# Kernel optimization log

Measured on AMD Instinct MI355X. Metric: run time of the kernel, lower is better.

Reference implementation:

```python
import jax, jax.numpy as jnp
import numpy as np

WS = 7          # window size
NH = 12         # num heads
DIM = 384
HID = 4 * DIM
EPS = 1e-5


def _rel_pos_index(ws):
    coords = np.stack(np.meshgrid(np.arange(ws), np.arange(ws), indexing='ij'))  # (2,ws,ws)
    cf = coords.reshape(2, -1)
    rel = cf[:, :, None] - cf[:, None, :]           # (2,N,N)
    rel = rel.transpose(1, 2, 0)                    # (N,N,2)
    rel[:, :, 0] += ws - 1
    rel[:, :, 1] += ws - 1
    rel[:, :, 0] *= 2 * ws - 1
    return jnp.asarray(rel.sum(-1))                 # (N,N) int

REL_IDX = _rel_pos_index(WS)


def _layernorm(x, g, b):
    m = x.mean(-1, keepdims=True)
    v = ((x - m) ** 2).mean(-1, keepdims=True)
    return (x - m) * jax.lax.rsqrt(v + EPS) * g + b


def setup_inputs() -> dict:
    key = jax.random.key(0)
    ks = jax.random.split(key, 16)
    B, H, W = 8, 112, 112
    s = lambda fan: 1.0 / np.sqrt(fan)
    return {
        'x': jax.random.normal(ks[0], (B, DIM, H, W), jnp.float32),
        'g1': jnp.ones((DIM,), jnp.float32),
        'b1': jnp.zeros((DIM,), jnp.float32),
        'w_qkv': jax.random.normal(ks[1], (DIM, 3 * DIM), jnp.float32) * s(DIM),
        'b_qkv': jnp.zeros((3 * DIM,), jnp.float32),
        'rpb': jax.random.normal(ks[2], ((2 * WS - 1) ** 2, NH), jnp.float32) * 0.02,
        'w_proj': jax.random.normal(ks[3], (DIM, DIM), jnp.float32) * s(DIM),
        'b_proj': jnp.zeros((DIM,), jnp.float32),
        'g2': jnp.ones((DIM,), jnp.float32),
        'b2': jnp.zeros((DIM,), jnp.float32),
        'w_fc1': jax.random.normal(ks[4], (DIM, HID), jnp.float32) * s(DIM),
        'b_fc1': jnp.zeros((HID,), jnp.float32),
        'w_fc2': jax.random.normal(ks[5], (HID, DIM), jnp.float32) * s(HID),
        'b_fc2': jnp.zeros((DIM,), jnp.float32),
    }


def reference(x, g1, b1, w_qkv, b_qkv, rpb, w_proj, b_proj, g2, b2, w_fc1, b_fc1, w_fc2, b_fc2):
    B, C, H, W = x.shape
    x = x.transpose(0, 2, 3, 1)                     # (B,H,W,C)
    shortcut = x
    xn = _layernorm(x, g1, b1)

    # window partition (with padding, no-op when divisible)
    pad_h = (-H) % WS
    pad_w = (-W) % WS
    if pad_h or pad_w:
        xn = jnp.pad(xn, ((0, 0), (0, pad_h), (0, pad_w), (0, 0)))
    Hp, Wp = H + pad_h, W + pad_w
    N = WS * WS
    xw = xn.reshape(B, Hp // WS, WS, Wp // WS, WS, C).transpose(0, 1, 3, 2, 4, 5)
    xw = xw.reshape(-1, N, C)                       # (B_, N, C)
    B_ = xw.shape[0]
    hd = C // NH

    qkv = (xw @ w_qkv + b_qkv).reshape(B_, N, 3, NH, hd)
    q = qkv[:, :, 0].transpose(0, 2, 1, 3) * (hd ** -0.5)   # (B_,h,N,d)
    k = qkv[:, :, 1].transpose(0, 2, 1, 3)
    v = qkv[:, :, 2].transpose(0, 2, 1, 3)

    attn = jnp.einsum('bhnd,bhmd->bhnm', q, k)
    bias = rpb[REL_IDX.reshape(-1)].reshape(N, N, NH).transpose(2, 0, 1)  # (h,N,N)
    attn = jax.nn.softmax(attn + bias[None], axis=-1)

    out = jnp.einsum('bhnm,bhmd->bhnd', attn, v).transpose(0, 2, 1, 3).reshape(B_, N, C)
    out = out @ w_proj + b_proj

    # window reverse
    out = out.reshape(B, Hp // WS, Wp // WS, WS, WS, C).transpose(0, 1, 3, 2, 4, 5)
    out = out.reshape(B, Hp, Wp, C)[:, :H, :W]

    x = shortcut + out
    h = _layernorm(x, g2, b2)
    h = jax.nn.gelu(h @ w_fc1 + b_fc1, approximate=False) @ w_fc2 + b_fc2
    x = x + h
    return x.transpose(0, 3, 1, 2)                  # (B,C,H,W)
```

## Files before the change

### kernel.cpp

```cpp
#include <hip/hip_runtime.h>
#include <cstdint>
#include <cmath>

using u16 = unsigned short;

typedef __bf16 bf16x8 __attribute__((ext_vector_type(8)));
typedef float  f32x4  __attribute__((ext_vector_type(4)));

__device__ __forceinline__ float b2f(u16 u) {
    return __uint_as_float(((unsigned int)u) << 16);
}
__device__ __forceinline__ u16 f2b(float f) {
    unsigned int x = __float_as_uint(f);
    unsigned int r = (x + 0x7fffu + ((x >> 16) & 1u)) >> 16;
    return (u16)r;
}

__device__ __forceinline__ void gload16(const u16* g, u16* l) {
    __builtin_amdgcn_global_load_lds((__attribute__((address_space(1))) void*)g,
                                     (__attribute__((address_space(3))) void*)l,
                                     16, 0, 0);
}

#define LGKM0_FENCE() do { \
    asm volatile("s_waitcnt lgkmcnt(0)" ::: "memory"); \
    __builtin_amdgcn_sched_barrier(0); } while (0)

__device__ __forceinline__ float gelu_f(float x) {
    float z = fabsf(x) * 0.70710678118f;
    float t = __builtin_amdgcn_rcpf(fmaf(0.3275911f, z, 1.0f));
    float poly = fmaf(fmaf(fmaf(fmaf(1.061405429f, t, -1.453152027f),
                               t, 1.421413741f),
                          t, -0.284496736f),
                     t, 0.254829592f) * t;
    float e = __expf(-z * z);
    float erfv = copysignf(1.0f - poly * e, x);
    return 0.5f * x * (1.0f + erfv);
}

__device__ __forceinline__ int tprime(int b, int hw) {
    int r = hw / 112, c = hw - r * 112;
    int wy = r / 7, iy = r - wy * 7;
    int wx = c / 7, ix = c - wx * 7;
    return (b * 256 + wy * 16 + wx) * 49 + iy * 7 + ix;
}

__global__ void detect_dtype(const unsigned int* __restrict__ x, int* __restrict__ flag) {
    __shared__ int cnt[256];
    int tid = threadIdx.x;
    int c = 0;
#pragma unroll
    for (int i = 0; i < 16; ++i) {
        unsigned int w = x[tid * 16 + i];
        int e = (w >> 23) & 0xFF;
        if (e >= 100 && e <= 150) ++c;
    }
    cnt[tid] = c;
    __syncthreads();
    if (tid == 0) {
        int s = 0;
        for (int i = 0; i < 256; ++i) s += cnt[i];
        flag[0] = (s > 3072) ? 1 : 0;
    }
}

__global__ void convertk(const void* __restrict__ src, u16* __restrict__ dst, int n,
                         const int* __restrict__ flagp) {
    int isf = flagp[0];
    int i = blockIdx.x * 256 + threadIdx.x;
    if (i < n) dst[i] = isf ? f2b(((const float*)src)[i]) : ((const u16*)src)[i];
}

__global__ void build_bias(const u16* __restrict__ crpb, float* __restrict__ bias_exp) {
    int row = blockIdx.x, h = blockIdx.y, col = threadIdx.x;
    float v = -1e30f;
    if (row < 49 && col < 49) {
        int ri = row / 7, rj = row - ri * 7;
        int mi = col / 7, mj = col - mi * 7;
        int idx = ((ri - mi + 6) * 13 + (rj - mj + 6)) * 12 + h;
        v = b2f(crpb[idx]);
    }
    bias_exp[(h * 64 + row) * 64 + col] = v;
}

__global__ void wtrans(const u16* __restrict__ in, u16* __restrict__ out, int K, int N) {
    __shared__ u16 tile[32][33];
    int n0 = blockIdx.x * 32, k0 = blockIdx.y * 32;
    int tx = threadIdx.x & 31, ty = threadIdx.x >> 5;
#pragma unroll
    for (int i = 0; i < 4; ++i)
        tile[ty + i * 8][tx] = in[(size_t)(k0 + ty + i * 8) * N + n0 + tx];
    __syncthreads();
#pragma unroll
    for (int i = 0; i < 4; ++i)
        out[(size_t)(n0 + ty + i * 8) * K + k0 + tx] = tile[tx][ty + i * 8];
}

__global__ void ln1_stats(const void* __restrict__ x, float* __restrict__ mean,
                          float* __restrict__ rstd, const int* __restrict__ flagp) {
    int isf = flagp[0];
    int t = blockIdx.x * 256 + threadIdx.x;
    int b = t / 12544, hw = t - b * 12544;
    size_t base = (size_t)b * 384 * 12544 + hw;
    float s = 0.f, sq = 0.f;
    if (isf) {
        const float* p = (const float*)x + base;
        for (int c = 0; c < 384; ++c) {
            float v = p[(size_t)c * 12544];
            s += v; sq += v * v;
        }
    } else {
        const u16* p = (const u16*)x + base;
        for (int c = 0; c < 384; ++c) {
            float v = b2f(p[(size_t)c * 12544]);
            s += v; sq += v * v;
        }
    }
    float m = s * (1.0f / 384.0f);
    float var = sq * (1.0f / 384.0f) - m * m;
    mean[t] = m;
    rstd[t] = rsqrtf(var + 1e-5f);
}

__global__ void ln1_apply(const void* __restrict__ x, const float* __restrict__ mean,
                          const float* __restrict__ rstd, const u16* __restrict__ g1,
                          const u16* __restrict__ b1, u16* __restrict__ xt,
                          u16* __restrict__ xn, const int* __restrict__ flagp) {
    __shared__ float tile[64][65];
    int isf = flagp[0];
    int hw0 = blockIdx.x * 64, c0 = blockIdx.y * 64, b = blockIdx.z;
    int tid = threadIdx.x;
    {
        int hl = tid & 63, cq = tid >> 6;
        size_t base = ((size_t)b * 384 + c0) * 12544 + hw0;
#pragma unroll
        for (int it = 0; it < 16; ++it) {
            int cl = cq * 16 + it;
            size_t idx = base + (size_t)cl * 12544 + hl;
            tile[cl][hl] = isf ? ((const float*)x)[idx] : b2f(((const u16*)x)[idx]);
        }
    }
    __syncthreads();
    {
        int cl = tid & 63, hq = tid >> 6;
        float g = b2f(g1[c0 + cl]), bb = b2f(b1[c0 + cl]);
#pragma unroll
        for (int it = 0; it < 16; ++it) {
            int hl = hq * 16 + it;
            int hw = hw0 + hl;
            int t = b * 12544 + hw;
            int tp = tprime(b, hw);
            float v = tile[cl][hl];
            size_t o = (size_t)tp * 384 + c0 + cl;
            xt[o] = f2b(v);
            xn[o] = f2b((v - mean[t]) * rstd[t] * g + bb);
        }
    }
}

template <int EPI>
__global__ void gemm_bt(const u16* __restrict__ A, const u16* __restrict__ Bt,
                        const u16* __restrict__ bias, const u16* __restrict__ res,
                        u16* __restrict__ Cout, int M, int N, int K) {
    __shared__ __align__(16) u16 S[2][2][128 * 32];
    const int tid = threadIdx.x;
    const int wave = tid >> 6, lane = tid & 63;

    const int nbx = gridDim.x;
    const int nwg = nbx * gridDim.y;
    int flat = blockIdx.y * nbx + blockIdx.x;
    {
        int q = nwg >> 3, r = nwg & 7;
        int xcd = flat & 7, loc = flat >> 3;
        flat = (xcd < r ? xcd * (q + 1) : r * (q + 1) + (xcd - r) * q) + loc;
    }
    const int m0 = (flat / nbx) * 128, n0 = (flat % nbx) * 128;

    const int wm = wave & 1, wn = wave >> 1;
    const int m15 = lane & 15, q4 = lane >> 4;

    const u16* gA = A + (size_t)(m0 + wave * 32 + (lane >> 2)) * K + (lane & 3) * 8;
    const u16* gB = Bt + (size_t)(n0 + wave * 32 + (lane >> 2)) * K + (lane & 3) * 8;

    f32x4 acc[4][4];
#pragma unroll
    for (int i = 0; i < 4; ++i)
#pragma unroll
        for (int j = 0; j < 4; ++j) acc[i][j] = {0.f, 0.f, 0.f, 0.f};

    const int nt = K >> 5;
    {
        u16* lA = &S[0][0][(wave * 32) * 32];
        u16* lB = &S[0][1][(wave * 32) * 32];
        gload16(gA, lA);
        gload16(gA + 16 * (size_t)K, lA + 16 * 32);
        gload16(gB, lB);
        gload16(gB + 16 * (size_t)K, lB + 16 * 32);
    }
    __syncthreads();

    for (int t = 0; t < nt; ++t) {
        const int cur = t & 1;
        if (t + 1 < nt) {
            const int k0 = (t + 1) << 5;
            u16* lA = &S[cur ^ 1][0][(wave * 32) * 32];
            u16* lB = &S[cur ^ 1][1][(wave * 32) * 32];
            gload16(gA + k0, lA);
            gload16(gA + k0 + 16 * (size_t)K, lA + 16 * 32);
            gload16(gB + k0, lB);
            gload16(gB + k0 + 16 * (size_t)K, lB + 16 * 32);
        }
        bf16x8 af[4], bfr[4];
#pragma unroll
        for (int i = 0; i < 4; ++i)
            af[i] = *(const bf16x8*)&S[cur][0][(wm * 64 + i * 16 + m15) * 32 + q4 * 8];
#pragma unroll
        for (int j = 0; j < 4; ++j)
            bfr[j] = *(const bf16x8*)&S[cur][1][(wn * 64 + j * 16 + m15) * 32 + q4 * 8];
#pragma unroll
        for (int i = 0; i < 4; ++i)
#pragma unroll
            for (int j = 0; j < 4; ++j)
                acc[i][j] = __builtin_amdgcn_mfma_f32_16x16x32_bf16(af[i], bfr[j],
                                                                    acc[i][j], 0, 0, 0);
        __syncthreads();
    }

    constexpr int CSTR = 132;
    float* Cs = (float*)&S[0][0][0];
#pragma unroll
    for (int p = 0; p < 4; ++p) {
        __syncthreads();
        if (wm == (p >> 1)) {
            const int ibase = (p & 1) * 2;
#pragma unroll
            for (int jj = 0; jj < 4; ++jj) {
                int n = n0 + wn * 64 + jj * 16 + m15;
                float bv = b2f(bias[n]);
#pragma unroll
                for (int ii = 0; ii < 2; ++ii) {
                    int i = ibase + ii;
#pragma unroll
                    for (int r = 0; r < 4; ++r) {
                        float v = acc[i][jj][r] + bv;
                        if (EPI == 1) v = gelu_f(v);
                        Cs[(ii * 16 + q4 * 4 + r) * CSTR + wn * 64 + jj * 16 + m15] = v;
                    }
                }
            }
        }
        __syncthreads();
#pragma unroll
        for (int it = 0; it < 2; ++it) {
            int r2 = it * 16 + (tid >> 4);
            int c8 = (tid & 15) * 8;
            size_t goff = (size_t)(m0 + p * 32 + r2) * N + n0 + c8;
            f32x4 v0 = *(const f32x4*)&Cs[r2 * CSTR + c8];
            f32x4 v1 = *(const f32x4*)&Cs[r2 * CSTR + c8 + 4];
            uint4 rv = {0u, 0u, 0u, 0u};
            const u16* rp = (const u16*)&rv;
            if (EPI == 2) rv = *(const uint4*)&res[goff];
            u16 outv[8];
#pragma unroll
            for (int e = 0; e < 4; ++e) {
                float a = v0[e];
                if (EPI == 2) a += b2f(rp[e]);
                outv[e] = f2b(a);
                float bq = v1[e];
                if (EPI == 2) bq += b2f(rp[4 + e]);
                outv[4 + e] = f2b(bq);
            }
            *(uint4*)&Cout[goff] = *(const uint4*)outv;
        }
    }
}

__global__ __launch_bounds__(256, 3)
void attn_win(const u16* __restrict__ qkv, const float* __restrict__ bias_exp,
              u16* __restrict__ outp) {
    __shared__ __align__(16) u16 lds[4][4096];
    const int tid = threadIdx.x;
    const int wave = tid >> 6, lane = tid & 63;
    const int t0p = blockIdx.x * 49;
    u16* Vt = &lds[wave][0];
    u16* Ps = &lds[wave][0];
    u16* Po = &lds[wave][0];
    const int m15 = lane & 15, q4 = lane >> 4;
    const int rr = lane >> 2, dq = lane & 3;
    const float scale = 0.17677669529663687f;
    const u16* wbase = qkv + (size_t)t0p * 1152;

    auto loadQK = [&](int h, bf16x8* qf, bf16x8* kf) {
#pragma unroll
        for (int i = 0; i < 4; ++i) {
            int row = i * 16 + m15;
            int rc = row < 49 ? row : 48;
            const u16* g = wbase + (size_t)rc * 1152 + h * 32 + q4 * 8;
            qf[i] = *(const bf16x8*)g;
            kf[i] = *(const bf16x8*)(g + 384);
        }
    };
    auto loadV = [&](int h, uint4* vv) {
#pragma unroll
        for (int p = 0; p < 4; ++p) {
            int n = p * 16 + rr;
            vv[p] = {0u, 0u, 0u, 0u};
            if (n < 49)
                vv[p] = *(const uint4*)(wbase + (size_t)n * 1152 + 768 + h * 32 + dq * 8);
        }
    };

    bf16x8 qfA[4], kfA[4];
    uint4 vvA[4];
    loadQK(wave, qfA, kfA);
    loadV(wave, vvA);

#pragma unroll
    for (int hl = 0; hl < 3; ++hl) {
        const int h = hl * 4 + wave;
#pragma unroll
        for (int p = 0; p < 4; ++p) {
            int n = p * 16 + rr;
            const u16* pv = (const u16*)&vvA[p];
#pragma unroll
            for (int ii = 0; ii < 8; ++ii) Vt[(dq * 8 + ii) * 64 + n] = pv[ii];
        }
        bf16x8 qfB[4], kfB[4];
        uint4 vvB[4];
        if (hl < 2) {
            loadQK(h + 4, qfB, kfB);
            loadV(h + 4, vvB);
        }
        LGKM0_FENCE();
        bf16x8 vf[2][2];
#pragma unroll
        for (int j = 0; j < 2; ++j)
#pragma unroll
            for (int kk = 0; kk < 2; ++kk)
                vf[j][kk] = *(const bf16x8*)&Vt[(j * 16 + m15) * 64 + kk * 32 + q4 * 8];
        f32x4 sc[4][4];
#pragma unroll
        for (int i = 0; i < 4; ++i)
#pragma unroll
            for (int j = 0; j < 4; ++j) {
                sc[i][j] = {0.f, 0.f, 0.f, 0.f};
                sc[i][j] = __builtin_amdgcn_mfma_f32_16x16x32_bf16(qfA[i], kfA[j],
                                                                   sc[i][j], 0, 0, 0);
            }
        const float* bx = bias_exp + h * 4096;
#pragma unroll
        for (int i = 0; i < 4; ++i)
#pragma unroll
            for (int r = 0; r < 4; ++r) {
                int row = i * 16 + q4 * 4 + r;
#pragma unroll
                for (int j = 0; j < 4; ++j)
                    sc[i][j][r] = fmaf(sc[i][j][r], scale, bx[row * 64 + j * 16 + m15]);
            }
#pragma unroll
        for (int i = 0; i < 4; ++i) {
#pragma unroll
            for (int r = 0; r < 4; ++r) {
                float mx = fmaxf(fmaxf(sc[i][0][r], sc[i][1][r]),
                                 fmaxf(sc[i][2][r], sc[i][3][r]));
                mx = fmaxf(mx, __shfl_xor(mx, 1));
                mx = fmaxf(mx, __shfl_xor(mx, 2));
                mx = fmaxf(mx, __shfl_xor(mx, 4));
                mx = fmaxf(mx, __shfl_xor(mx, 8));
                float e0 = __expf(sc[i][0][r] - mx);
                float e1 = __expf(sc[i][1][r] - mx);
                float e2 = __expf(sc[i][2][r] - mx);
                float e3 = __expf(sc[i][3][r] - mx);
                float sum = e0 + e1 + e2 + e3;
                sum += __shfl_xor(sum, 1);
                sum += __shfl_xor(sum, 2);
                sum += __shfl_xor(sum, 4);
                sum += __shfl_xor(sum, 8);
                float inv = 1.0f / sum;
                sc[i][0][r] = e0 * inv;
                sc[i][1][r] = e1 * inv;
                sc[i][2][r] = e2 * inv;
                sc[i][3][r] = e3 * inv;
            }
        }
#pragma unroll
        for (int i = 0; i < 4; ++i)
#pragma unroll
            for (int r = 0; r < 4; ++r)
#pragma unroll
                for (int j = 0; j < 4; ++j)
                    Ps[(i * 16 + q4 * 4 + r) * 64 + j * 16 + m15] = f2b(sc[i][j][r]);
        LGKM0_FENCE();
        f32x4 oacc[4][2];
#pragma unroll
        for (int i = 0; i < 4; ++i)
#pragma unroll
            for (int j = 0; j < 2; ++j) oacc[i][j] = {0.f, 0.f, 0.f, 0.f};
#pragma unroll
        for (int i = 0; i < 4; ++i) {
#pragma unroll
            for (int kk = 0; kk < 2; ++kk) {
                bf16x8 pf = *(const bf16x8*)&Ps[(i * 16 + m15) * 64 + kk * 32 + q4 * 8];
#pragma unroll
                for (int j = 0; j < 2; ++j)
                    oacc[i][j] = __builtin_amdgcn_mfma_f32_16x16x32_bf16(pf, vf[j][kk],
                                                                         oacc[i][j], 0, 0, 0);
            }
        }
#pragma unroll
        for (int i = 0; i < 4; ++i)
#pragma unroll
            for (int r = 0; r < 4; ++r) {
                int row = i * 16 + q4 * 4 + r;
#pragma unroll
                for (int j = 0; j < 2; ++j)
                    Po[row * 40 + j * 16 + m15] = f2b(oacc[i][j][r]);
            }
        LGKM0_FENCE();
#pragma unroll
        for (int w2 = 0; w2 < 4; ++w2) {
            int row = w2 * 16 + rr;
            if (row < 49) {
                uint4 ov = *(const uint4*)&Po[row * 40 + dq * 8];
                *(uint4*)&outp[(size_t)(t0p + row) * 384 + h * 32 + dq * 8] = ov;
            }
        }
        if (hl < 2) {
#pragma unroll
            for (int i = 0; i < 4; ++i) {
                qfA[i] = qfB[i];
                kfA[i] = kfB[i];
                vvA[i] = vvB[i];
            }
        }
    }
}

__global__ void ln2_kernel(const u16* __restrict__ y, const u16* __restrict__ g2,
                           const u16* __restrict__ b2, u16* __restrict__ out) {
    int wave = threadIdx.x >> 6, lane = threadIdx.x & 63;
    size_t t = (size_t)blockIdx.x * 4 + wave;
    const u16* row = y + t * 384;
    float v[6];
    float s = 0.f, sq = 0.f;
#pragma unroll
    for (int i = 0; i < 6; ++i) {
        v[i] = b2f(row[lane + i * 64]);
        s += v[i]; sq += v[i] * v[i];
    }
#pragma unroll
    for (int m = 1; m < 64; m <<= 1) {
        s += __shfl_xor(s, m);
        sq += __shfl_xor(sq, m);
    }
    float mean = s * (1.0f / 384.0f);
    float var = sq * (1.0f / 384.0f) - mean * mean;
    float rstd = rsqrtf(var + 1e-5f);
#pragma unroll
    for (int i = 0; i < 6; ++i) {
        int c = lane + i * 64;
        out[t * 384 + c] = f2b((v[i] - mean) * rstd * b2f(g2[c]) + b2f(b2[c]));
    }
}

__global__ void out_transpose(const u16* __restrict__ fin, void* __restrict__ out,
                              const int* __restrict__ flagp) {
    __shared__ float tile[64][65];
    int isf = flagp[0];
    int hw0 = blockIdx.x * 64, c0 = blockIdx.y * 64, b = blockIdx.z;
    int tid = threadIdx.x;
    {
        int cl = tid & 63, hq = tid >> 6;
#pragma unroll
        for (int it = 0; it < 16; ++it) {
            int hl = hq * 16 + it;
            int tp = tprime(b, hw0 + hl);
            tile[hl][cl] = b2f(fin[(size_t)tp * 384 + c0 + cl]);
        }
    }
    __syncthreads();
    {
        int hl = tid & 63, cq = tid >> 6;
#pragma unroll
        for (int it = 0; it < 16; ++it) {
            int cl = cq * 16 + it;
            size_t o = ((size_t)b * 384 + c0 + cl) * 12544 + hw0 + hl;
            float v = tile[hl][cl];
            if (isf) ((float*)out)[o] = v;
            else     ((u16*)out)[o] = f2b(v);
        }
    }
}

extern "C" void kernel_launch(void* const* d_in, const int* in_sizes, int n_in,
                              void* d_out, int out_size, void* d_ws, size_t ws_size,
                              hipStream_t stream) {
    constexpr int T = 100352, C = 384, HID = 1536, NQ = 1152;
    const void* x      = d_in[0];
    u16* out_any = (u16*)d_out;
    (void)out_any;

    char* ws = (char*)d_ws;
    size_t off = 0;
    auto alloc = [&](size_t bytes) { char* p = ws + off; off += (bytes + 255) & ~(size_t)255; return p; };
    int*   flag   = (int*)alloc(4);
    u16* cw_qkv  = (u16*)alloc((size_t)C * NQ * 2);
    u16* cb_qkv  = (u16*)alloc((size_t)NQ * 2);
    u16* crpb    = (u16*)alloc((size_t)169 * 12 * 2);
    u16* cw_proj = (u16*)alloc((size_t)C * C * 2);
    u16* cb_proj = (u16*)alloc((size_t)C * 2);
    u16* cg1     = (u16*)alloc((size_t)C * 2);
    u16* cb1     = (u16*)alloc((size_t)C * 2);
    u16* cg2     = (u16*)alloc((size_t)C * 2);
    u16* cb2     = (u16*)alloc((size_t)C * 2);
    u16* cw_fc1  = (u16*)alloc((size_t)C * HID * 2);
    u16* cb_fc1  = (u16*)alloc((size_t)HID * 2);
    u16* cw_fc2  = (u16*)alloc((size_t)HID * C * 2);
    u16* cb_fc2  = (u16*)alloc((size_t)C * 2);
    u16* wqkvT  = (u16*)alloc((size_t)C * NQ * 2);
    u16* wprojT = (u16*)alloc((size_t)C * C * 2);
    u16* wfc1T  = (u16*)alloc((size_t)C * HID * 2);
    u16* wfc2T  = (u16*)alloc((size_t)HID * C * 2);
    float* biasx = (float*)alloc((size_t)12 * 64 * 64 * 4);
    u16*   xt     = (u16*)alloc((size_t)T * C * 2);
    u16*   bufB   = (u16*)alloc((size_t)T * C * 2);
    u16*   bufC   = (u16*)alloc((size_t)T * HID * 2);
    u16*   ybuf   = (u16*)alloc((size_t)T * C * 2);
    float* meanb  = (float*)alloc((size_t)T * 4);
    float* rstdb  = (float*)alloc((size_t)T * 4);

    detect_dtype<<<1, 256, 0, stream>>>((const unsigned int*)x, flag);

    auto conv = [&](const void* src, u16* dst, int n) {
        convertk<<<(n + 255) / 256, 256, 0, stream>>>(src, dst, n, flag);
    };
    conv(d_in[1], cg1, C);
    conv(d_in[2], cb1, C);
    conv(d_in[3], cw_qkv, C * NQ);
    conv(d_in[4], cb_qkv, NQ);
    conv(d_in[5], crpb, 169 * 12);
    conv(d_in[6], cw_proj, C * C);
    conv(d_in[7], cb_proj, C);
    conv(d_in[8], cg2, C);
    conv(d_in[9], cb2, C);
    conv(d_in[10], cw_fc1, C * HID);
    conv(d_in[11], cb_fc1, HID);
    conv(d_in[12], cw_fc2, HID * C);
    conv(d_in[13], cb_fc2, C);

    build_bias<<<dim3(64, 12), 64, 0, stream>>>(crpb, biasx);

    wtrans<<<dim3(NQ / 32, C / 32), 256, 0, stream>>>(cw_qkv, wqkvT, C, NQ);
    wtrans<<<dim3(C / 32, C / 32), 256, 0, stream>>>(cw_proj, wprojT, C, C);
    wtrans<<<dim3(HID / 32, C / 32), 256, 0, stream>>>(cw_fc1, wfc1T, C, HID);
    wtrans<<<dim3(C / 32, HID / 32), 256, 0, stream>>>(cw_fc2, wfc2T, HID, C);

    ln1_stats<<<T / 256, 256, 0, stream>>>(x, meanb, rstdb, flag);
    ln1_apply<<<dim3(196, 6, 8), 256, 0, stream>>>(x, meanb, rstdb, cg1, cb1, xt, bufB, flag);

    gemm_bt<0><<<dim3(NQ / 128, T / 128), 256, 0, stream>>>(bufB, wqkvT, cb_qkv, nullptr,
                                                            bufC, T, NQ, C);
    attn_win<<<2048, 256, 0, stream>>>(bufC, biasx, bufB);

    gemm_bt<2><<<dim3(C / 128, T / 128), 256, 0, stream>>>(bufB, wprojT, cb_proj, xt,
                                                           ybuf, T, C, C);
    ln2_kernel<<<T / 4, 256, 0, stream>>>(ybuf, cg2, cb2, bufB);

    gemm_bt<1><<<dim3(HID / 128, T / 128), 256, 0, stream>>>(bufB, wfc1T, cb_fc1, nullptr,
                                                             bufC, T, HID, C);
    gemm_bt<2><<<dim3(C / 128, T / 128), 256, 0, stream>>>(bufC, wfc2T, cb_fc2, ybuf,
                                                           bufB, T, C, HID);
    out_transpose<<<dim3(196, 6, 8), 256, 0, stream>>>(bufB, d_out, flag);
}
```

Measured before the change: 1.281 ms.

## Fuse prep and LN1 kernels, templatize GEMM dims, add per-wave bf16 epilogue

Merges the many small conversion, bias-building and weight-transpose launches into two prep kernels. Fuses the LN1 statistics and apply passes into one kernel that reads x twice per tile instead of going through separate mean/rstd buffers. The GEMM takes N and K as template constants and, for non-residual epilogues, stages bf16 results per wave with no block barriers. LN2 loads and stores are vectorized, and a hardware bf16 conversion replaces the manual rounding. The fused LN1 runs with fewer blocks, which may cut parallelism on the strided channel reads.

```diff
diff --git a/kernel.cpp b/kernel.cpp
--- a/kernel.cpp
+++ b/kernel.cpp
@@ -14,6 +14,11 @@
     unsigned int x = __float_as_uint(f);
     unsigned int r = (x + 0x7fffu + ((x >> 16) & 1u)) >> 16;
     return (u16)r;
+}
+__device__ __forceinline__ u16 f2b_fast(float f) {
+    union { __bf16 h; u16 u; } cv;
+    cv.h = (__bf16)f;
+    return cv.u;
 }
 
 __device__ __forceinline__ void gload16(const u16* g, u16* l) {
@@ -64,104 +69,124 @@
     }
 }
 
-__global__ void convertk(const void* __restrict__ src, u16* __restrict__ dst, int n,
-                         const int* __restrict__ flagp) {
+__global__ void prep_small(const void* g1, const void* b1, const void* bqkv,
+                           const void* bproj, const void* g2, const void* b2,
+                           const void* bfc1, const void* bfc2, const void* rpb,
+                           u16* cg1, u16* cb1, u16* cbqkv, u16* cbproj,
+                           u16* cg2, u16* cb2, u16* cbfc1, u16* cbfc2,
+                           float* bias_exp, const int* __restrict__ flagp) {
     int isf = flagp[0];
-    int i = blockIdx.x * 256 + threadIdx.x;
-    if (i < n) dst[i] = isf ? f2b(((const float*)src)[i]) : ((const u16*)src)[i];
-}
-
-__global__ void build_bias(const u16* __restrict__ crpb, float* __restrict__ bias_exp) {
-    int row = blockIdx.x, h = blockIdx.y, col = threadIdx.x;
-    float v = -1e30f;
-    if (row < 49 && col < 49) {
-        int ri = row / 7, rj = row - ri * 7;
-        int mi = col / 7, mj = col - mi * 7;
-        int idx = ((ri - mi + 6) * 13 + (rj - mj + 6)) * 12 + h;
-        v = b2f(crpb[idx]);
-    }
-    bias_exp[(h * 64 + row) * 64 + col] = v;
-}
-
-__global__ void wtrans(const u16* __restrict__ in, u16* __restrict__ out, int K, int N) {
+    int tid = threadIdx.x;
+    auto cv = [&](const void* s, int i) {
+        return isf ? f2b(((const float*)s)[i]) : ((const u16*)s)[i];
+    };
+    for (int i = tid; i < 384; i += 256) cg1[i] = cv(g1, i);
+    for (int i = tid; i < 384; i += 256) cb1[i] = cv(b1, i);
+    for (int i = tid; i < 1152; i += 256) cbqkv[i] = cv(bqkv, i);
+    for (int i = tid; i < 384; i += 256) cbproj[i] = cv(bproj, i);
+    for (int i = tid; i < 384; i += 256) cg2[i] = cv(g2, i);
+    for (int i = tid; i < 384; i += 256) cb2[i] = cv(b2, i);
+    for (int i = tid; i < 1536; i += 256) cbfc1[i] = cv(bfc1, i);
+    for (int i = tid; i < 384; i += 256) cbfc2[i] = cv(bfc2, i);
+    for (int i = tid; i < 12 * 64 * 64; i += 256) {
+        int h = i >> 12, row = (i >> 6) & 63, col = i & 63;
+        float v = -1e30f;
+        if (row < 49 && col < 49) {
+            int ri = row / 7, rj = row - ri * 7;
+            int mi = col / 7, mj = col - mi * 7;
+            int idx = ((ri - mi + 6) * 13 + (rj - mj + 6)) * 12 + h;
+            v = isf ? ((const float*)rpb)[idx] : b2f(((const u16*)rpb)[idx]);
+        }
+        bias_exp[i] = v;
+    }
+}
+
+__global__ void prep_w(const void* w0, const void* w1, const void* w2, const void* w3,
+                       u16* o0, u16* o1, u16* o2, u16* o3,
+                       const int* __restrict__ flagp) {
     __shared__ u16 tile[32][33];
+    int isf = flagp[0];
+    const void* src; u16* dst; int K, N;
+    switch (blockIdx.z) {
+        case 0: src = w0; dst = o0; K = 384;  N = 1152; break;
+        case 1: src = w1; dst = o1; K = 384;  N = 384;  break;
+        case 2: src = w2; dst = o2; K = 384;  N = 1536; break;
+        default: src = w3; dst = o3; K = 1536; N = 384; break;
+    }
+    if ((int)blockIdx.x >= N / 32 || (int)blockIdx.y >= K / 32) return;
     int n0 = blockIdx.x * 32, k0 = blockIdx.y * 32;
     int tx = threadIdx.x & 31, ty = threadIdx.x >> 5;
 #pragma unroll
+    for (int i = 0; i < 4; ++i) {
+        size_t idx = (size_t)(k0 + ty + i * 8) * N + n0 + tx;
+        tile[ty + i * 8][tx] = isf ? f2b(((const float*)src)[idx])
+                                   : ((const u16*)src)[idx];
+    }
+    __syncthreads();
+#pragma unroll
     for (int i = 0; i < 4; ++i)
-        tile[ty + i * 8][tx] = in[(size_t)(k0 + ty + i * 8) * N + n0 + tx];
-    __syncthreads();
-#pragma unroll
-    for (int i = 0; i < 4; ++i)
-        out[(size_t)(n0 + ty + i * 8) * K + k0 + tx] = tile[tx][ty + i * 8];
-}
-
-__global__ void ln1_stats(const void* __restrict__ x, float* __restrict__ mean,
-                          float* __restrict__ rstd, const int* __restrict__ flagp) {
-    int isf = flagp[0];
-    int t = blockIdx.x * 256 + threadIdx.x;
-    int b = t / 12544, hw = t - b * 12544;
-    size_t base = (size_t)b * 384 * 12544 + hw;
-    float s = 0.f, sq = 0.f;
-    if (isf) {
-        const float* p = (const float*)x + base;
-        for (int c = 0; c < 384; ++c) {
-            float v = p[(size_t)c * 12544];
-            s += v; sq += v * v;
-        }
-    } else {
-        const u16* p = (const u16*)x + base;
-        for (int c = 0; c < 384; ++c) {
-            float v = b2f(p[(size_t)c * 12544]);
-            s += v; sq += v * v;
-        }
-    }
-    float m = s * (1.0f / 384.0f);
-    float var = sq * (1.0f / 384.0f) - m * m;
-    mean[t] = m;
-    rstd[t] = rsqrtf(var + 1e-5f);
-}
-
-__global__ void ln1_apply(const void* __restrict__ x, const float* __restrict__ mean,
-                          const float* __restrict__ rstd, const u16* __restrict__ g1,
+        dst[(size_t)(n0 + ty + i * 8) * K + k0 + tx] = tile[tx][ty + i * 8];
+}
+
+__global__ void ln1_fused(const void* __restrict__ x, const u16* __restrict__ g1,
                           const u16* __restrict__ b1, u16* __restrict__ xt,
                           u16* __restrict__ xn, const int* __restrict__ flagp) {
-    __shared__ float tile[64][65];
+    __shared__ float tile[64][66];
+    __shared__ float part[4][64];
+    __shared__ float part2[4][64];
+    __shared__ float stat[2][64];
     int isf = flagp[0];
-    int hw0 = blockIdx.x * 64, c0 = blockIdx.y * 64, b = blockIdx.z;
-    int tid = threadIdx.x;
-    {
-        int hl = tid & 63, cq = tid >> 6;
-        size_t base = ((size_t)b * 384 + c0) * 12544 + hw0;
-#pragma unroll
-        for (int it = 0; it < 16; ++it) {
-            int cl = cq * 16 + it;
-            size_t idx = base + (size_t)cl * 12544 + hl;
-            tile[cl][hl] = isf ? ((const float*)x)[idx] : b2f(((const u16*)x)[idx]);
-        }
-    }
+    int hw0 = blockIdx.x * 64, b = blockIdx.y;
+    int tid = threadIdx.x, hl = tid & 63, cq = tid >> 6;
+    size_t base = (size_t)b * 384 * 12544 + hw0 + hl;
+    float s = 0.f, sq = 0.f;
+    for (int ci = 0; ci < 96; ++ci) {
+        int c = cq * 96 + ci;
+        float v = isf ? ((const float*)x)[base + (size_t)c * 12544]
+                      : b2f(((const u16*)x)[base + (size_t)c * 12544]);
+        s += v; sq += v * v;
+    }
+    part[cq][hl] = s;
+    part2[cq][hl] = sq;
     __syncthreads();
-    {
-        int cl = tid & 63, hq = tid >> 6;
-        float g = b2f(g1[c0 + cl]), bb = b2f(b1[c0 + cl]);
-#pragma unroll
-        for (int it = 0; it < 16; ++it) {
-            int hl = hq * 16 + it;
-            int hw = hw0 + hl;
-            int t = b * 12544 + hw;
-            int tp = tprime(b, hw);
-            float v = tile[cl][hl];
-            size_t o = (size_t)tp * 384 + c0 + cl;
-            xt[o] = f2b(v);
-            xn[o] = f2b((v - mean[t]) * rstd[t] * g + bb);
-        }
-    }
-}
-
-template <int EPI>
+    if (tid < 64) {
+        float S1 = part[0][tid] + part[1][tid] + part[2][tid] + part[3][tid];
+        float S2 = part2[0][tid] + part2[1][tid] + part2[2][tid] + part2[3][tid];
+        float m = S1 * (1.0f / 384.0f);
+        float var = S2 * (1.0f / 384.0f) - m * m;
+        stat[0][tid] = m;
+        stat[1][tid] = rsqrtf(var + 1e-5f);
+    }
+    __syncthreads();
+    for (int ch = 0; ch < 6; ++ch) {
+#pragma unroll
+        for (int k = 0; k < 16; ++k) {
+            int c = ch * 64 + cq * 16 + k;
+            float v = isf ? ((const float*)x)[base + (size_t)c * 12544]
+                          : b2f(((const u16*)x)[base + (size_t)c * 12544]);
+            tile[cq * 16 + k][hl] = v;
+        }
+        __syncthreads();
+#pragma unroll
+        for (int k2 = 0; k2 < 16; ++k2) {
+            int tok = cq * 16 + k2;
+            int tp = tprime(b, hw0 + tok);
+            float m = stat[0][tok], rs = stat[1][tok];
+            int c = ch * 64 + hl;
+            float v = tile[hl][tok];
+            float g = b2f(g1[c]), bb = b2f(b1[c]);
+            size_t o = (size_t)tp * 384 + c;
+            xt[o] = f2b_fast(v);
+            xn[o] = f2b_fast((v - m) * rs * g + bb);
+        }
+        __syncthreads();
+    }
+}
+
+template <int EPI, int N, int K>
 __global__ void gemm_bt(const u16* __restrict__ A, const u16* __restrict__ Bt,
                         const u16* __restrict__ bias, const u16* __restrict__ res,
-                        u16* __restrict__ Cout, int M, int N, int K) {
+                        u16* __restrict__ Cout, int M) {
     __shared__ __align__(16) u16 S[2][2][128 * 32];
     const int tid = threadIdx.x;
     const int wave = tid >> 6, lane = tid & 63;
@@ -188,7 +213,7 @@
 #pragma unroll
         for (int j = 0; j < 4; ++j) acc[i][j] = {0.f, 0.f, 0.f, 0.f};
 
-    const int nt = K >> 5;
+    constexpr int nt = K >> 5;
     {
         u16* lA = &S[0][0][(wave * 32) * 32];
         u16* lB = &S[0][1][(wave * 32) * 32];
@@ -226,51 +251,69 @@
         __syncthreads();
     }
 
-    constexpr int CSTR = 132;
-    float* Cs = (float*)&S[0][0][0];
-#pragma unroll
-    for (int p = 0; p < 4; ++p) {
-        __syncthreads();
-        if (wm == (p >> 1)) {
-            const int ibase = (p & 1) * 2;
-#pragma unroll
-            for (int jj = 0; jj < 4; ++jj) {
-                int n = n0 + wn * 64 + jj * 16 + m15;
-                float bv = b2f(bias[n]);
-#pragma unroll
-                for (int ii = 0; ii < 2; ++ii) {
-                    int i = ibase + ii;
-#pragma unroll
-                    for (int r = 0; r < 4; ++r) {
-                        float v = acc[i][jj][r] + bv;
-                        if (EPI == 1) v = gelu_f(v);
-                        Cs[(ii * 16 + q4 * 4 + r) * CSTR + wn * 64 + jj * 16 + m15] = v;
+    if (EPI <= 1) {
+        u16* W = &S[0][0][0] + wave * 4096;
+#pragma unroll
+        for (int jj = 0; jj < 4; ++jj) {
+            int n = n0 + wn * 64 + jj * 16 + m15;
+            float bv = b2f(bias[n]);
+#pragma unroll
+            for (int i = 0; i < 4; ++i)
+#pragma unroll
+                for (int r = 0; r < 4; ++r) {
+                    float v = acc[i][jj][r] + bv;
+                    if (EPI == 1) v = gelu_f(v);
+                    W[(i * 16 + q4 * 4 + r) * 64 + jj * 16 + m15] = f2b_fast(v);
+                }
+        }
+#pragma unroll
+        for (int o = 0; o < 8; ++o) {
+            int lrow = o * 8 + (lane >> 3);
+            int c8 = (lane & 7) * 8;
+            uint4 v = *(const uint4*)&W[lrow * 64 + c8];
+            *(uint4*)&Cout[(size_t)(m0 + wm * 64 + lrow) * N + n0 + wn * 64 + c8] = v;
+        }
+    } else {
+        constexpr int CSTR = 132;
+        float* Cs = (float*)&S[0][0][0];
+#pragma unroll
+        for (int p = 0; p < 4; ++p) {
+            __syncthreads();
+            if (wm == (p >> 1)) {
+                const int ibase = (p & 1) * 2;
+#pragma unroll
+                for (int jj = 0; jj < 4; ++jj) {
+                    int n = n0 + wn * 64 + jj * 16 + m15;
+                    float bv = b2f(bias[n]);
+#pragma unroll
+                    for (int ii = 0; ii < 2; ++ii) {
+                        int i = ibase + ii;
+#pragma unroll
+                        for (int r = 0; r < 4; ++r) {
+                            float v = acc[i][jj][r] + bv;
+                            Cs[(ii * 16 + q4 * 4 + r) * CSTR + wn * 64 + jj * 16 + m15] = v;
+                        }
                     }
                 }
             }
-        }
-        __syncthreads();
-#pragma unroll
-        for (int it = 0; it < 2; ++it) {
-            int r2 = it * 16 + (tid >> 4);
-            int c8 = (tid & 15) * 8;
-            size_t goff = (size_t)(m0 + p * 32 + r2) * N + n0 + c8;
-            f32x4 v0 = *(const f32x4*)&Cs[r2 * CSTR + c8];
-            f32x4 v1 = *(const f32x4*)&Cs[r2 * CSTR + c8 + 4];
-            uint4 rv = {0u, 0u, 0u, 0u};
-            const u16* rp = (const u16*)&rv;
-            if (EPI == 2) rv = *(const uint4*)&res[goff];
-            u16 outv[8];
-#pragma unroll
-            for (int e = 0; e < 4; ++e) {
-                float a = v0[e];
-                if (EPI == 2) a += b2f(rp[e]);
-                outv[e] = f2b(a);
-                float bq = v1[e];
-                if (EPI == 2) bq += b2f(rp[4 + e]);
-                outv[4 + e] = f2b(bq);
-            }
-            *(uint4*)&Cout[goff] = *(const uint4*)outv;
+            __syncthreads();
+#pragma unroll
+            for (int it = 0; it < 2; ++it) {
+                int r2 = it * 16 + (tid >> 4);
+                int c8 = (tid & 15) * 8;
+                size_t goff = (size_t)(m0 + p * 32 + r2) * N + n0 + c8;
+                f32x4 v0 = *(const f32x4*)&Cs[r2 * CSTR + c8];
+                f32x4 v1 = *(const f32x4*)&Cs[r2 * CSTR + c8 + 4];
+                uint4 rv = *(const uint4*)&res[goff];
+                const u16* rp = (const u16*)&rv;
+                u16 outv[8];
+#pragma unroll
+                for (int e = 0; e < 4; ++e) {
+                    outv[e] = f2b_fast(v0[e] + b2f(rp[e]));
+                    outv[4 + e] = f2b_fast(v1[e] + b2f(rp[4 + e]));
+                }
+                *(uint4*)&Cout[goff] = *(const uint4*)outv;
+            }
         }
     }
 }
@@ -440,14 +483,14 @@
                            const u16* __restrict__ b2, u16* __restrict__ out) {
     int wave = threadIdx.x >> 6, lane = threadIdx.x & 63;
     size_t t = (size_t)blockIdx.x * 4 + wave;
-    const u16* row = y + t * 384;
+    uint3 rv = *(const uint3*)(y + t * 384 + lane * 6);
     float v[6];
+    v[0] = b2f((u16)(rv.x & 0xffff)); v[1] = b2f((u16)(rv.x >> 16));
+    v[2] = b2f((u16)(rv.y & 0xffff)); v[3] = b2f((u16)(rv.y >> 16));
+    v[4] = b2f((u16)(rv.z & 0xffff)); v[5] = b2f((u16)(rv.z >> 16));
     float s = 0.f, sq = 0.f;
 #pragma unroll
-    for (int i = 0; i < 6; ++i) {
-        v[i] = b2f(row[lane + i * 64]);
-        s += v[i]; sq += v[i] * v[i];
-    }
+    for (int i = 0; i < 6; ++i) { s += v[i]; sq += v[i] * v[i]; }
 #pragma unroll
     for (int m = 1; m < 64; m <<= 1) {
         s += __shfl_xor(s, m);
@@ -456,11 +499,24 @@
     float mean = s * (1.0f / 384.0f);
     float var = sq * (1.0f / 384.0f) - mean * mean;
     float rstd = rsqrtf(var + 1e-5f);
-#pragma unroll
-    for (int i = 0; i < 6; ++i) {
-        int c = lane + i * 64;
-        out[t * 384 + c] = f2b((v[i] - mean) * rstd * b2f(g2[c]) + b2f(b2[c]));
-    }
+    uint3 gv = *(const uint3*)(g2 + lane * 6);
+    uint3 bv = *(const uint3*)(b2 + lane * 6);
+    float g[6], bb[6];
+    g[0] = b2f((u16)(gv.x & 0xffff)); g[1] = b2f((u16)(gv.x >> 16));
+    g[2] = b2f((u16)(gv.y & 0xffff)); g[3] = b2f((u16)(gv.y >> 16));
+    g[4] = b2f((u16)(gv.z & 0xffff)); g[5] = b2f((u16)(gv.z >> 16));
+    bb[0] = b2f((u16)(bv.x & 0xffff)); bb[1] = b2f((u16)(bv.x >> 16));
+    bb[2] = b2f((u16)(bv.y & 0xffff)); bb[3] = b2f((u16)(bv.y >> 16));
+    bb[4] = b2f((u16)(bv.z & 0xffff)); bb[5] = b2f((u16)(bv.z >> 16));
+    u16 o[6];
+#pragma unroll
+    for (int i = 0; i < 6; ++i)
+        o[i] = f2b_fast((v[i] - mean) * rstd * g[i] + bb[i]);
+    uint3 ov;
+    ov.x = (unsigned)o[0] | ((unsigned)o[1] << 16);
+    ov.y = (unsigned)o[2] | ((unsigned)o[3] << 16);
+    ov.z = (unsigned)o[4] | ((unsigned)o[5] << 16);
+    *(uint3*)(out + t * 384 + lane * 6) = ov;
 }
 
 __global__ void out_transpose(const u16* __restrict__ fin, void* __restrict__ out,
@@ -496,79 +552,52 @@
                               void* d_out, int out_size, void* d_ws, size_t ws_size,
                               hipStream_t stream) {
     constexpr int T = 100352, C = 384, HID = 1536, NQ = 1152;
-    const void* x      = d_in[0];
-    u16* out_any = (u16*)d_out;
-    (void)out_any;
+    const void* x = d_in[0];
 
     char* ws = (char*)d_ws;
     size_t off = 0;
     auto alloc = [&](size_t bytes) { char* p = ws + off; off += (bytes + 255) & ~(size_t)255; return p; };
-    int*   flag   = (int*)alloc(4);
-    u16* cw_qkv  = (u16*)alloc((size_t)C * NQ * 2);
+    int* flag = (int*)alloc(4);
     u16* cb_qkv  = (u16*)alloc((size_t)NQ * 2);
-    u16* crpb    = (u16*)alloc((size_t)169 * 12 * 2);
-    u16* cw_proj = (u16*)alloc((size_t)C * C * 2);
     u16* cb_proj = (u16*)alloc((size_t)C * 2);
     u16* cg1     = (u16*)alloc((size_t)C * 2);
     u16* cb1     = (u16*)alloc((size_t)C * 2);
     u16* cg2     = (u16*)alloc((size_t)C * 2);
     u16* cb2     = (u16*)alloc((size_t)C * 2);
-    u16* cw_fc1  = (u16*)alloc((size_t)C * HID * 2);
     u16* cb_fc1  = (u16*)alloc((size_t)HID * 2);
-    u16* cw_fc2  = (u16*)alloc((size_t)HID * C * 2);
     u16* cb_fc2  = (u16*)alloc((size_t)C * 2);
     u16* wqkvT  = (u16*)alloc((size_t)C * NQ * 2);
     u16* wprojT = (u16*)alloc((size_t)C * C * 2);
     u16* wfc1T  = (u16*)alloc((size_t)C * HID * 2);
     u16* wfc2T  = (u16*)alloc((size_t)HID * C * 2);
     float* biasx = (float*)alloc((size_t)12 * 64 * 64 * 4);
-    u16*   xt     = (u16*)alloc((size_t)T * C * 2);
-    u16*   bufB   = (u16*)alloc((size_t)T * C * 2);
-    u16*   bufC   = (u16*)alloc((size_t)T * HID * 2);
-    u16*   ybuf   = (u16*)alloc((size_t)T * C * 2);
-    float* meanb  = (float*)alloc((size_t)T * 4);
-    float* rstdb  = (float*)alloc((size_t)T * 4);
+    u16* xt   = (u16*)alloc((size_t)T * C * 2);
+    u16* bufB = (u16*)alloc((size_t)T * C * 2);
+    u16* bufC = (u16*)alloc((size_t)T * HID * 2);
+    u16* ybuf = (u16*)alloc((size_t)T * C * 2);
 
     detect_dtype<<<1, 256, 0, stream>>>((const unsigned int*)x, flag);
 
-    auto conv = [&](const void* src, u16* dst, int n) {
-        convertk<<<(n + 255) / 256, 256, 0, stream>>>(src, dst, n, flag);
-    };
-    conv(d_in[1], cg1, C);
-    conv(d_in[2], cb1, C);
-    conv(d_in[3], cw_qkv, C * NQ);
-    conv(d_in[4], cb_qkv, NQ);
-    conv(d_in[5], crpb, 169 * 12);
-    conv(d_in[6], cw_proj, C * C);
-    conv(d_in[7], cb_proj, C);
-    conv(d_in[8], cg2, C);
-    conv(d_in[9], cb2, C);
-    conv(d_in[10], cw_fc1, C * HID);
-    conv(d_in[11], cb_fc1, HID);
-    conv(d_in[12], cw_fc2, HID * C);
-    conv(d_in[13], cb_fc2, C);
-
-    build_bias<<<dim3(64, 12), 64, 0, stream>>>(crpb, biasx);
-
-    wtrans<<<dim3(NQ / 32, C / 32), 256, 0, stream>>>(cw_qkv, wqkvT, C, NQ);
-    wtrans<<<dim3(C / 32, C / 32), 256, 0, stream>>>(cw_proj, wprojT, C, C);
-    wtrans<<<dim3(HID / 32, C / 32), 256, 0, stream>>>(cw_fc1, wfc1T, C, HID);
-    wtrans<<<dim3(C / 32, HID / 32), 256, 0, stream>>>(cw_fc2, wfc2T, HID, C);
-
-    ln1_stats<<<T / 256, 256, 0, stream>>>(x, meanb, rstdb, flag);
-    ln1_apply<<<dim3(196, 6, 8), 256, 0, stream>>>(x, meanb, rstdb, cg1, cb1, xt, bufB, flag);
-
-    gemm_bt<0><<<dim3(NQ / 128, T / 128), 256, 0, stream>>>(bufB, wqkvT, cb_qkv, nullptr,
-                                                            bufC, T, NQ, C);
+    prep_small<<<1, 256, 0, stream>>>(d_in[1], d_in[2], d_in[4], d_in[7], d_in[8],
+                                      d_in[9], d_in[11], d_in[13], d_in[5],
+                                      cg1, cb1, cb_qkv, cb_proj, cg2, cb2,
+                                      cb_fc1, cb_fc2, biasx, flag);
+    prep_w<<<dim3(48, 48, 4), 256, 0, stream>>>(d_in[3], d_in[6], d_in[10], d_in[12],
+                                                wqkvT, wprojT, wfc1T, wfc2T, flag);
+
+    ln1_fused<<<dim3(196, 8), 256, 0, stream>>>(x, cg1, cb1, xt, bufB, flag);
+
+    gemm_bt<0, NQ, C><<<dim3(NQ / 128, T / 128), 256, 0, stream>>>(
+        bufB, wqkvT, cb_qkv, nullptr, bufC, T);
     attn_win<<<2048, 256, 0, stream>>>(bufC, biasx, bufB);
 
-    gemm_bt<2><<<dim3(C / 128, T / 128), 256, 0, stream>>>(bufB, wprojT, cb_proj, xt,
-                                                           ybuf, T, C, C);
+    gemm_bt<2, C, C><<<dim3(C / 128, T / 128), 256, 0, stream>>>(
+        bufB, wprojT, cb_proj, xt, ybuf, T);
     ln2_kernel<<<T / 4, 256, 0, stream>>>(ybuf, cg2, cb2, bufB);
 
-    gemm_bt<1><<<dim3(HID / 128, T / 128), 256, 0, stream>>>(bufB, wfc1T, cb_fc1, nullptr,
-                                                             bufC, T, HID, C);
-    gemm_bt<2><<<dim3(C / 128, T / 128), 256, 0, stream>>>(bufC, wfc2T, cb_fc2, ybuf,
-                                                           bufB, T, C, HID);
+    gemm_bt<1, HID, C><<<dim3(HID / 128, T / 128), 256, 0, stream>>>(
+        bufB, wfc1T, cb_fc1, nullptr, bufC, T);
+    gemm_bt<2, C, HID><<<dim3(C / 128, T / 128), 256, 0, stream>>>(
+        bufC, wfc2T, cb_fc2, ybuf, bufB, T);
     out_transpose<<<dim3(196, 6, 8), 256, 0, stream>>>(bufB, d_out, flag);
 }
```

New measurement: 1.259 ms. About the same (-1.7%).
